# Optimization experiments

Hardware: AMD Instinct MI355X
Metric: run time of the kernel (lower is better)

Reference implementation:

```python
import jax, jax.numpy as jnp
import numpy as np

STATE_DIM = 512
HIDDEN = 256
ACTION = 8
BATCH = 32768
LN_EPS = 1e-5


def setup_inputs() -> dict:
    key = jax.random.key(0)
    ks = jax.random.split(key, 24)
    s = 0.02
    inp = {
        'initial_state': jax.random.normal(ks[0], (BATCH, STATE_DIM), jnp.float32),
        'final_state': jax.random.normal(ks[1], (BATCH, STATE_DIM), jnp.float32),
        'horizon': 10,
        # fc: Linear(1024->256), LayerNorm(256), ReLU, Linear(256->256), ReLU
        'W1': jax.random.normal(ks[2], (HIDDEN, 2 * STATE_DIM), jnp.float32) * s,
        'b1': jnp.zeros((HIDDEN,), jnp.float32),
        'ln_g': jnp.ones((HIDDEN,), jnp.float32),
        'ln_b': jnp.zeros((HIDDEN,), jnp.float32),
        'W2': jax.random.normal(ks[3], (HIDDEN, HIDDEN), jnp.float32) * s,
        'b2': jnp.zeros((HIDDEN,), jnp.float32),
        # GRU layer 0 (input=ACTION) and layer 1 (input=HIDDEN)
        'Wih0': jax.random.normal(ks[4], (3 * HIDDEN, ACTION), jnp.float32) * s,
        'Whh0': jax.random.normal(ks[5], (3 * HIDDEN, HIDDEN), jnp.float32) * s,
        'bih0': jnp.zeros((3 * HIDDEN,), jnp.float32),
        'bhh0': jnp.zeros((3 * HIDDEN,), jnp.float32),
        'Wih1': jax.random.normal(ks[6], (3 * HIDDEN, HIDDEN), jnp.float32) * s,
        'Whh1': jax.random.normal(ks[7], (3 * HIDDEN, HIDDEN), jnp.float32) * s,
        'bih1': jnp.zeros((3 * HIDDEN,), jnp.float32),
        'bhh1': jnp.zeros((3 * HIDDEN,), jnp.float32),
        # fc_action: 256 -> 8
        'Wa': jax.random.normal(ks[8], (ACTION, HIDDEN), jnp.float32) * s,
        'ba': jnp.zeros((ACTION,), jnp.float32),
        # fc_init_hidden: 256 -> 512
        'Winit': jax.random.normal(ks[9], (2 * HIDDEN, HIDDEN), jnp.float32) * s,
        'binit': jnp.zeros((2 * HIDDEN,), jnp.float32),
    }
    return inp


def _gru_cell(x, h, Wih, Whh, bih, bhh):
    # torch.nn.GRU cell: gates ordered [r, z, n]
    gi = x @ Wih.T + bih              # [B, 3H]
    gh = h @ Whh.T + bhh              # [B, 3H]
    i_r, i_z, i_n = jnp.split(gi, 3, axis=-1)
    h_r, h_z, h_n = jnp.split(gh, 3, axis=-1)
    r = jax.nn.sigmoid(i_r + h_r)
    z = jax.nn.sigmoid(i_z + h_z)
    n = jnp.tanh(i_n + r * h_n)
    return (1.0 - z) * n + z * h


def reference(initial_state, final_state, horizon, W1, b1, ln_g, ln_b, W2, b2,
              Wih0, Whh0, bih0, bhh0, Wih1, Whh1, bih1, bhh1, Wa, ba, Winit, binit):
    B = initial_state.shape[0]
    combined = jnp.concatenate([initial_state, final_state], axis=-1)  # [B, 2*state]
    h = combined @ W1.T + b1
    mu = jnp.mean(h, axis=-1, keepdims=True)
    var = jnp.var(h, axis=-1, keepdims=True)
    h = (h - mu) * jax.lax.rsqrt(var + LN_EPS) * ln_g + ln_b
    h = jax.nn.relu(h)
    h = jax.nn.relu(h @ W2.T + b2)    # [B, H]

    # Replicates torch .view(2, B, H) on a [B, 2H] tensor (row-major reshape)
    hidden = jnp.reshape(h @ Winit.T + binit, (2, B, HIDDEN))
    h0, h1 = hidden[0], hidden[1]
    a0 = jnp.zeros((B, ACTION), initial_state.dtype)

    def step(carry, _):
        h0, h1, a = carry
        h0n = _gru_cell(a, h0, Wih0, Whh0, bih0, bhh0)
        h1n = _gru_cell(h0n, h1, Wih1, Whh1, bih1, bhh1)
        logits = h1n @ Wa.T + ba       # [B, A]
        a_next = jax.nn.softmax(logits, axis=-1)
        return (h0n, h1n, a_next), logits

    _, logits_seq = jax.lax.scan(step, (h0, h1, a0), None, length=horizon)
    return jnp.transpose(logits_seq, (1, 0, 2))  # [B, horizon, A]
```

## Files before the change

### kernel.cpp

```cpp
#include <hip/hip_runtime.h>


#define HS 264
#define HR 256

typedef __attribute__((ext_vector_type(8))) short short8;
typedef __attribute__((ext_vector_type(4))) float fvec4;

__device__ __forceinline__ float bf2f(unsigned short u) {
    union { unsigned int u; float f; } x; x.u = ((unsigned int)u) << 16; return x.f;
}
__device__ __forceinline__ unsigned short f2bf(float f) {
    union { float f; unsigned int u; } x; x.f = f;
    unsigned int r = x.u + 0x7fffu + ((x.u >> 16) & 1u);
    return (unsigned short)(r >> 16);
}
__device__ __forceinline__ float sigm(float x)   { return __builtin_amdgcn_rcpf(1.f + __expf(-x)); }
__device__ __forceinline__ float tanh_f(float x) { return 2.f * __builtin_amdgcn_rcpf(1.f + __expf(-2.f * x)) - 1.f; }

__device__ __forceinline__ short8 ld8(const unsigned short* p) {
    return *reinterpret_cast<const short8*>(p);
}
__device__ __forceinline__ fvec4 mfma16(short8 a, short8 b, fvec4 c) {
    return __builtin_amdgcn_mfma_f32_16x16x32_bf16(a, b, c, 0, 0, 0);
}
__device__ __forceinline__ fvec4 splat4(float v) {
    fvec4 r = {v, v, v, v}; return r;
}
__device__ __forceinline__ int swz(int row, int k) {
    return row * HR + (k ^ ((row & 7) << 3));
}

__device__ __forceinline__ int packoff(int e, int K) {
    const int n = e / K, k = e % K;
    return (((n >> 4) * (K >> 5) + (k >> 5)) << 9)
         + (((((k >> 3) & 3) << 4) | (n & 15)) << 3) + (k & 7);
}

__global__ __launch_bounds__(256) void k_prep(
    const float* __restrict__ W1, const float* __restrict__ W2,
    const float* __restrict__ Winit, const float* __restrict__ Wih0,
    const float* __restrict__ Whh0, const float* __restrict__ Wih1,
    const float* __restrict__ Whh1, const float* __restrict__ Wa,
    unsigned short* __restrict__ wb)
{
    int i = blockIdx.x * 256 + threadIdx.x;
    if (i >= 1056768) return;
    float v; int dst;
    if (i < 262144) {
        v = W1[i];                dst = packoff(i, 1024);
    } else if (i < 327680) {
        int e = i - 262144;  v = W2[e];    dst = 262144 + packoff(e, 256);
    } else if (i < 458752) {
        int e = i - 327680;  v = Winit[e]; dst = 327680 + packoff(e, 256);
    } else if (i < 464896) {
        v = Wih0[i - 458752];     dst = i;
    } else if (i < 661504) {
        int e = i - 464896;  v = Whh0[e];  dst = 464896 + packoff(e, 256);
    } else if (i < 858112) {
        int e = i - 661504;  v = Wih1[e];  dst = 661504 + packoff(e, 256);
    } else if (i < 1054720) {
        int e = i - 858112;  v = Whh1[e];  dst = 858112 + packoff(e, 256);
    } else {
        v = Wa[i - 1054720];      dst = i;
    }
    wb[dst] = f2bf(v);
}

__global__ __launch_bounds__(512, 2) void k_encode(
    const float* __restrict__ ini, const float* __restrict__ fin,
    const unsigned short* __restrict__ W1b, const float* __restrict__ b1,
    const float* __restrict__ lng, const float* __restrict__ lnb,
    const unsigned short* __restrict__ W2b, const float* __restrict__ b2,
    const unsigned short* __restrict__ Winitb, const float* __restrict__ binit,
    unsigned short* __restrict__ h0g, unsigned short* __restrict__ h1g)
{
    __shared__ unsigned short hb[64 * HS];
    __shared__ unsigned short at[2][64 * 40];
    __shared__ float ps[64][8][2];
    __shared__ float st[64][2];
    const int tid = threadIdx.x, lane = tid & 63, w = tid >> 6;
    const int l15 = lane & 15, q = lane >> 4;
    const int rows0 = blockIdx.x * 64;
    const int c0 = w * 32;
    const fvec4 fz = {0.f, 0.f, 0.f, 0.f};

    const int srow = tid >> 3, sseg = (tid & 7) * 4;

    fvec4 acc[4][2];
#pragma unroll
    for (int rt = 0; rt < 4; ++rt) { acc[rt][0] = fz; acc[rt][1] = fz; }
    {
        const float* src0 = ini + (rows0 + srow) * 512 + sseg;
        fvec4 v = *reinterpret_cast<const fvec4*>(src0);
        union { unsigned short s[4]; unsigned long long u; } p;
        p.s[0] = f2bf(v[0]); p.s[1] = f2bf(v[1]); p.s[2] = f2bf(v[2]); p.s[3] = f2bf(v[3]);
        *reinterpret_cast<unsigned long long*>(&at[0][srow * 40 + sseg]) = p.u;
    }
    __syncthreads();
#pragma unroll 1
    for (int kc = 0; kc < 32; ++kc) {
        const int buf = kc & 1;
        if (kc < 31) {
            const int k0 = (kc + 1) * 32 + sseg;
            const float* src = (k0 < 512) ? (ini + (rows0 + srow) * 512 + k0)
                                          : (fin + (rows0 + srow) * 512 + (k0 - 512));
            fvec4 v = *reinterpret_cast<const fvec4*>(src);
            union { unsigned short s[4]; unsigned long long u; } p;
            p.s[0] = f2bf(v[0]); p.s[1] = f2bf(v[1]); p.s[2] = f2bf(v[2]); p.s[3] = f2bf(v[3]);
            *reinterpret_cast<unsigned long long*>(&at[buf ^ 1][srow * 40 + sseg]) = p.u;
        }
        short8 b8a = ld8(W1b + (((w * 2 + 0) * 32 + kc) * 64 + lane) * 8);
        short8 b8b = ld8(W1b + (((w * 2 + 1) * 32 + kc) * 64 + lane) * 8);
        short8 a8[4];
#pragma unroll
        for (int rt = 0; rt < 4; ++rt)
            a8[rt] = ld8(&at[buf][(rt * 16 + l15) * 40 + q * 8]);
#pragma unroll
        for (int rt = 0; rt < 4; ++rt) {
            acc[rt][0] = mfma16(a8[rt], b8a, acc[rt][0]);
            acc[rt][1] = mfma16(a8[rt], b8b, acc[rt][1]);
        }
        __syncthreads();
    }
    float bv[2] = { b1[c0 + l15], b1[c0 + 16 + l15] };
#pragma unroll
    for (int rt = 0; rt < 4; ++rt)
#pragma unroll
        for (int r = 0; r < 4; ++r) {
            float s = 0.f, s2 = 0.f;
#pragma unroll
            for (int ct = 0; ct < 2; ++ct) {
                float v = acc[rt][ct][r] + bv[ct];
                acc[rt][ct][r] = v;
                s += v; s2 += v * v;
            }
#pragma unroll
            for (int off = 1; off < 16; off <<= 1) {
                s  += __shfl_xor(s,  off, 64);
                s2 += __shfl_xor(s2, off, 64);
            }
            if (l15 == 0) {
                int row = rt * 16 + q * 4 + r;
                ps[row][w][0] = s; ps[row][w][1] = s2;
            }
        }
    __syncthreads();
    if (tid < 64) {
        float s = 0.f, s2 = 0.f;
#pragma unroll
        for (int j = 0; j < 8; ++j) { s += ps[tid][j][0]; s2 += ps[tid][j][1]; }
        float mu = s * (1.f / 256.f);
        float var = s2 * (1.f / 256.f) - mu * mu;
        st[tid][0] = mu; st[tid][1] = rsqrtf(var + 1e-5f);
    }
    __syncthreads();
    {
        float gv[2]  = { lng[c0 + l15], lng[c0 + 16 + l15] };
        float bbv[2] = { lnb[c0 + l15], lnb[c0 + 16 + l15] };
#pragma unroll
        for (int rt = 0; rt < 4; ++rt)
#pragma unroll
            for (int ct = 0; ct < 2; ++ct)
#pragma unroll
                for (int r = 0; r < 4; ++r) {
                    int row = rt * 16 + q * 4 + r;
                    float v = (acc[rt][ct][r] - st[row][0]) * st[row][1] * gv[ct] + bbv[ct];
                    v = fmaxf(v, 0.f);
                    hb[row * HS + c0 + ct * 16 + l15] = f2bf(v);
                }
    }
    __syncthreads();
    fvec4 acc2[4][2];
#pragma unroll
    for (int rt = 0; rt < 4; ++rt) { acc2[rt][0] = fz; acc2[rt][1] = fz; }
#pragma unroll 2
    for (int kc = 0; kc < 8; ++kc) {
        const int k0 = kc * 32 + q * 8;
        short8 a8[4];
#pragma unroll
        for (int rt = 0; rt < 4; ++rt) a8[rt] = ld8(hb + (rt * 16 + l15) * HS + k0);
#pragma unroll
        for (int ct = 0; ct < 2; ++ct) {
            short8 b8 = ld8(W2b + (((w * 2 + ct) * 8 + kc) * 64 + lane) * 8);
#pragma unroll
            for (int rt = 0; rt < 4; ++rt) acc2[rt][ct] = mfma16(a8[rt], b8, acc2[rt][ct]);
        }
    }
    {
        float b2v[2] = { b2[c0 + l15], b2[c0 + 16 + l15] };
        unsigned short stg[4][2][4];
#pragma unroll
        for (int rt = 0; rt < 4; ++rt)
#pragma unroll
            for (int ct = 0; ct < 2; ++ct)
#pragma unroll
                for (int r = 0; r < 4; ++r)
                    stg[rt][ct][r] = f2bf(fmaxf(acc2[rt][ct][r] + b2v[ct], 0.f));
        __syncthreads();
#pragma unroll
        for (int rt = 0; rt < 4; ++rt)
#pragma unroll
            for (int ct = 0; ct < 2; ++ct)
#pragma unroll
                for (int r = 0; r < 4; ++r)
                    hb[(rt * 16 + q * 4 + r) * HS + c0 + ct * 16 + l15] = stg[rt][ct][r];
    }
    __syncthreads();
    fvec4 a3[4][4];
#pragma unroll
    for (int rt = 0; rt < 4; ++rt)
#pragma unroll
        for (int ct = 0; ct < 4; ++ct) a3[rt][ct] = fz;
#pragma unroll 1
    for (int kc = 0; kc < 8; ++kc) {
        const int k0 = kc * 32 + q * 8;
        short8 a8[4];
#pragma unroll
        for (int rt = 0; rt < 4; ++rt) a8[rt] = ld8(hb + (rt * 16 + l15) * HS + k0);
#pragma unroll
        for (int ct = 0; ct < 4; ++ct) {
            short8 b8 = ld8(Winitb + (((w * 4 + ct) * 8 + kc) * 64 + lane) * 8);
#pragma unroll
            for (int rt = 0; rt < 4; ++rt) a3[rt][ct] = mfma16(a8[rt], b8, a3[rt][ct]);
        }
    }
    const int c0i = w * 64;
#pragma unroll
    for (int ct = 0; ct < 4; ++ct) {
        const int j = c0i + ct * 16 + l15;
        const float bz = binit[j];
        const int half = j >> 8, cc = j & 255;
#pragma unroll
        for (int rt = 0; rt < 4; ++rt)
#pragma unroll
            for (int r = 0; r < 4; ++r) {
                const int i = rows0 + rt * 16 + q * 4 + r;
                const unsigned short v = f2bf(a3[rt][ct][r] + bz);
                if (i < 16384) h0g[(2 * i + half) * 256 + cc] = v;
                else           h1g[(2 * (i - 16384) + half) * 256 + cc] = v;
            }
    }
}

__global__ __launch_bounds__(512, 2) void k_roll(
    const unsigned short* __restrict__ h0g, const unsigned short* __restrict__ h1g,
    const unsigned short* __restrict__ Wih0b, const unsigned short* __restrict__ Whh0b,
    const unsigned short* __restrict__ Wih1b, const unsigned short* __restrict__ Whh1b,
    const unsigned short* __restrict__ Wab,
    const float* __restrict__ bih0, const float* __restrict__ bhh0,
    const float* __restrict__ bih1, const float* __restrict__ bhh1,
    const float* __restrict__ ba, float* __restrict__ out)
{
    __shared__ unsigned short h0sb[2][64 * HR];
    __shared__ unsigned short h1sb[2][64 * HR];
    __shared__ unsigned short avs[64 * 8];
    __shared__ float ldsb[2048];
    const int tid = threadIdx.x, lane = tid & 63, w = tid >> 6;
    const int l15 = lane & 15, q = lane >> 4;
    const int rows0 = blockIdx.x * 64;
    const int cb = w * 32;
    const fvec4 fz = {0.f, 0.f, 0.f, 0.f};
    const short8 z8 = {0,0,0,0,0,0,0,0};

    for (int it = tid; it < 64 * 32; it += 512) {
        const int row = it >> 5, g = (it & 31) * 8;
        const int d = swz(row, g);
        *reinterpret_cast<short8*>(&h0sb[0][d]) = ld8(h0g + (rows0 + row) * 256 + g);
        *reinterpret_cast<short8*>(&h1sb[0][d]) = ld8(h1g + (rows0 + row) * 256 + g);
    }
    if (tid < 256) {
        const int j = tid;
        ldsb[j]       = bih0[j] + bhh0[j];
        ldsb[256 + j] = bih0[256 + j] + bhh0[256 + j];
        ldsb[512 + j] = bih0[512 + j];
        ldsb[768 + j] = bhh0[512 + j];
    } else {
        const int j = tid - 256;
        ldsb[1024 + j] = bih1[j] + bhh1[j];
        ldsb[1280 + j] = bih1[256 + j] + bhh1[256 + j];
        ldsb[1536 + j] = bih1[512 + j];
        ldsb[1792 + j] = bhh1[512 + j];
    }
    const float bav = ba[l15 & 7];
    __syncthreads();

    for (int t = 0; t < 10; ++t) {
        const int cur = t & 1, nxt = cur ^ 1;
        const unsigned short* h0c = h0sb[cur];
        unsigned short*       h0n = h0sb[nxt];
        const unsigned short* h1c = h1sb[cur];
        unsigned short*       h1n = h1sb[nxt];
#pragma unroll 1
        for (int p = 0; p < 2; ++p) {
            const int c = cb + p * 16 + l15;
            fvec4 aR[4], aZ[4], aNi[4], aNh[4];
            {
                const float vr = ldsb[c],       vz = ldsb[256 + c];
                const float vi = ldsb[512 + c], vh = ldsb[768 + c];
#pragma unroll
                for (int rt = 0; rt < 4; ++rt) {
                    aR[rt]  = splat4(vr);
                    aZ[rt]  = splat4(vz);
                    aNi[rt] = splat4(vi);
                    aNh[rt] = splat4(vh);
                }
            }
            if (t > 0) {
                const unsigned short* wp = Wih0b + c * 8;
                const short8 wr = ld8(wp);
                const short8 wz = ld8(wp + 2048);
                const short8 wn = ld8(wp + 4096);
#pragma unroll
                for (int rt = 0; rt < 4; ++rt) {
                    short8 v = ld8(avs + (rt * 16 + l15) * 8);
                    const short8 av = (q == 0) ? v : z8;
                    aR[rt]  = mfma16(av, wr, aR[rt]);
                    aZ[rt]  = mfma16(av, wz, aZ[rt]);
                    aNi[rt] = mfma16(av, wn, aNi[rt]);
                }
            }
#pragma unroll 4
            for (int kc = 0; kc < 8; ++kc) {
                const int k0 = kc * 32 + q * 8;
                const unsigned short* wp =
                    Whh0b + ((((w * 2 + p) * 8 + kc) * 64 + lane) * 8);
                const short8 wr = ld8(wp);
                const short8 wz = ld8(wp + 65536);
                const short8 wn = ld8(wp + 131072);
#pragma unroll
                for (int rt = 0; rt < 4; ++rt) {
                    const short8 ah = ld8(h0c + swz(rt * 16 + l15, k0));
                    aR[rt]  = mfma16(ah, wr, aR[rt]);
                    aZ[rt]  = mfma16(ah, wz, aZ[rt]);
                    aNh[rt] = mfma16(ah, wn, aNh[rt]);
                }
            }
#pragma unroll
            for (int rt = 0; rt < 4; ++rt)
#pragma unroll
                for (int r = 0; r < 4; ++r) {
                    const int row = rt * 16 + q * 4 + r;
                    const float hold = bf2f(h0c[swz(row, c)]);
                    const float rr = sigm(aR[rt][r]);
                    const float zz = sigm(aZ[rt][r]);
                    const float nn = tanh_f(aNi[rt][r] + rr * aNh[rt][r]);
                    h0n[swz(row, c)] = f2bf((1.f - zz) * nn + zz * hold);
                }
        }
        __syncthreads();
#pragma unroll 1
        for (int p = 0; p < 2; ++p) {
            const int c = cb + p * 16 + l15;
            fvec4 aR[4], aZ[4], aNi[4], aNh[4];
            {
                const float vr = ldsb[1024 + c], vz = ldsb[1280 + c];
                const float vi = ldsb[1536 + c], vh = ldsb[1792 + c];
#pragma unroll
                for (int rt = 0; rt < 4; ++rt) {
                    aR[rt]  = splat4(vr);
                    aZ[rt]  = splat4(vz);
                    aNi[rt] = splat4(vi);
                    aNh[rt] = splat4(vh);
                }
            }
#pragma unroll 4
            for (int kc = 0; kc < 8; ++kc) {
                const int k0 = kc * 32 + q * 8;
                const unsigned short* wi =
                    Wih1b + ((((w * 2 + p) * 8 + kc) * 64 + lane) * 8);
                const short8 wir = ld8(wi);
                const short8 wiz = ld8(wi + 65536);
                const short8 win = ld8(wi + 131072);
#pragma unroll
                for (int rt = 0; rt < 4; ++rt) {
                    const short8 ai = ld8(h0n + swz(rt * 16 + l15, k0));
                    aR[rt]  = mfma16(ai, wir, aR[rt]);
                    aZ[rt]  = mfma16(ai, wiz, aZ[rt]);
                    aNi[rt] = mfma16(ai, win, aNi[rt]);
                }
            }
#pragma unroll 4
            for (int kc = 0; kc < 8; ++kc) {
                const int k0 = kc * 32 + q * 8;
                const unsigned short* wh =
                    Whh1b + ((((w * 2 + p) * 8 + kc) * 64 + lane) * 8);
                const short8 whr = ld8(wh);
                const short8 whz = ld8(wh + 65536);
                const short8 whn = ld8(wh + 131072);
#pragma unroll
                for (int rt = 0; rt < 4; ++rt) {
                    const short8 ah = ld8(h1c + swz(rt * 16 + l15, k0));
                    aR[rt]  = mfma16(ah, whr, aR[rt]);
                    aZ[rt]  = mfma16(ah, whz, aZ[rt]);
                    aNh[rt] = mfma16(ah, whn, aNh[rt]);
                }
            }
#pragma unroll
            for (int rt = 0; rt < 4; ++rt)
#pragma unroll
                for (int r = 0; r < 4; ++r) {
                    const int row = rt * 16 + q * 4 + r;
                    const float hold = bf2f(h1c[swz(row, c)]);
                    const float rr = sigm(aR[rt][r]);
                    const float zz = sigm(aZ[rt][r]);
                    const float nn = tanh_f(aNi[rt][r] + rr * aNh[rt][r]);
                    h1n[swz(row, c)] = f2bf((1.f - zz) * nn + zz * hold);
                }
        }
        __syncthreads();
        if (w < 4) {
            fvec4 f = fz;
#pragma unroll 1
            for (int kc = 0; kc < 8; ++kc) {
                const int k0 = kc * 32 + q * 8;
                short8 a8 = ld8(h1n + swz(w * 16 + l15, k0));
                short8 b8 = ld8(Wab + (l15 & 7) * 256 + k0);
                f = mfma16(a8, b8, f);
            }
#pragma unroll
            for (int r = 0; r < 4; ++r) {
                float s = f[r] + bav;
                float m = s;
                m = fmaxf(m, __shfl_xor(m, 1, 64));
                m = fmaxf(m, __shfl_xor(m, 2, 64));
                m = fmaxf(m, __shfl_xor(m, 4, 64));
                float e = __expf(s - m);
                float se = e;
                se += __shfl_xor(se, 1, 64);
                se += __shfl_xor(se, 2, 64);
                se += __shfl_xor(se, 4, 64);
                if (l15 < 8) {
                    const int lrow = w * 16 + q * 4 + r;
                    out[(rows0 + lrow) * 80 + t * 8 + l15] = s;
                    avs[lrow * 8 + l15] = f2bf(e * __builtin_amdgcn_rcpf(se));
                }
            }
        }
        __syncthreads();
    }
}

extern "C" void kernel_launch(void* const* d_in, const int* in_sizes, int n_in,
                              void* d_out, int out_size, void* d_ws, size_t ws_size,
                              hipStream_t stream)
{
    const float* ini   = (const float*)d_in[0];
    const float* fin   = (const float*)d_in[1];
    const float* W1    = (const float*)d_in[3];
    const float* b1    = (const float*)d_in[4];
    const float* lng   = (const float*)d_in[5];
    const float* lnb   = (const float*)d_in[6];
    const float* W2    = (const float*)d_in[7];
    const float* b2    = (const float*)d_in[8];
    const float* Wih0  = (const float*)d_in[9];
    const float* Whh0  = (const float*)d_in[10];
    const float* bih0  = (const float*)d_in[11];
    const float* bhh0  = (const float*)d_in[12];
    const float* Wih1  = (const float*)d_in[13];
    const float* Whh1  = (const float*)d_in[14];
    const float* bih1  = (const float*)d_in[15];
    const float* bhh1  = (const float*)d_in[16];
    const float* Wa    = (const float*)d_in[17];
    const float* ba    = (const float*)d_in[18];
    const float* Winit = (const float*)d_in[19];
    const float* binit = (const float*)d_in[20];
    float* out = (float*)d_out;

    char* ws = (char*)d_ws;
    unsigned short* wb     = (unsigned short*)ws;
    unsigned short* W1b    = wb;
    unsigned short* W2b    = wb + 262144;
    unsigned short* Winitb = wb + 327680;
    unsigned short* Wih0b  = wb + 458752;
    unsigned short* Whh0b  = wb + 464896;
    unsigned short* Wih1b  = wb + 661504;
    unsigned short* Whh1b  = wb + 858112;
    unsigned short* Wab    = wb + 1054720;
    unsigned short* h0g = (unsigned short*)(ws + 2113536);
    unsigned short* h1g = (unsigned short*)(ws + 18890752);

    k_prep<<<dim3(4128), dim3(256), 0, stream>>>(W1, W2, Winit, Wih0, Whh0, Wih1, Whh1, Wa, wb);
    k_encode<<<dim3(512), dim3(512), 0, stream>>>(ini, fin, W1b, b1, lng, lnb, W2b, b2,
                                                  Winitb, binit, h0g, h1g);
    k_roll<<<dim3(512), dim3(512), 0, stream>>>(h0g, h1g, Wih0b, Whh0b, Wih1b, Whh1b, Wab,
                                                bih0, bhh0, bih1, bhh1, ba, out);
}
```

Before: 724.1 us.

## Double k_roll waves to 16 per block and use padded LDS rows

The GRU rollout kernel now runs 1024 threads per block, so each wave owns one 16-column slice instead of looping over two. This raises waves per CU for latency hiding and shortens each wave's serial work between barriers. The XOR-swizzled hidden-state LDS layout is replaced by rows padded to 264 elements, which removes the swizzle index arithmetic but may change the bank-conflict pattern. The tighter launch bounds cap registers per thread, which risks spills given the 16 MFMA accumulators each wave holds.

```diff
diff --git a/kernel.cpp b/kernel.cpp
--- a/kernel.cpp
+++ b/kernel.cpp
@@ -2,7 +2,6 @@
 
 
 #define HS 264
-#define HR 256
 
 typedef __attribute__((ext_vector_type(8))) short short8;
 typedef __attribute__((ext_vector_type(4))) float fvec4;
@@ -26,9 +25,6 @@
 }
 __device__ __forceinline__ fvec4 splat4(float v) {
     fvec4 r = {v, v, v, v}; return r;
-}
-__device__ __forceinline__ int swz(int row, int k) {
-    return row * HR + (k ^ ((row & 7) << 3));
 }
 
 __device__ __forceinline__ int packoff(int e, int K) {
@@ -243,7 +239,7 @@
     }
 }
 
-__global__ __launch_bounds__(512, 2) void k_roll(
+__global__ __launch_bounds__(1024, 4) void k_roll(
     const unsigned short* __restrict__ h0g, const unsigned short* __restrict__ h1g,
     const unsigned short* __restrict__ Wih0b, const unsigned short* __restrict__ Whh0b,
     const unsigned short* __restrict__ Wih1b, const unsigned short* __restrict__ Whh1b,
@@ -252,22 +248,21 @@
     const float* __restrict__ bih1, const float* __restrict__ bhh1,
     const float* __restrict__ ba, float* __restrict__ out)
 {
-    __shared__ unsigned short h0sb[2][64 * HR];
-    __shared__ unsigned short h1sb[2][64 * HR];
+    __shared__ unsigned short h0sb[2][64 * HS];
+    __shared__ unsigned short h1sb[2][64 * HS];
     __shared__ unsigned short avs[64 * 8];
     __shared__ float ldsb[2048];
     const int tid = threadIdx.x, lane = tid & 63, w = tid >> 6;
     const int l15 = lane & 15, q = lane >> 4;
     const int rows0 = blockIdx.x * 64;
-    const int cb = w * 32;
+    const int c = w * 16 + l15;
     const fvec4 fz = {0.f, 0.f, 0.f, 0.f};
     const short8 z8 = {0,0,0,0,0,0,0,0};
 
-    for (int it = tid; it < 64 * 32; it += 512) {
+    for (int it = tid; it < 64 * 32; it += 1024) {
         const int row = it >> 5, g = (it & 31) * 8;
-        const int d = swz(row, g);
-        *reinterpret_cast<short8*>(&h0sb[0][d]) = ld8(h0g + (rows0 + row) * 256 + g);
-        *reinterpret_cast<short8*>(&h1sb[0][d]) = ld8(h1g + (rows0 + row) * 256 + g);
+        *reinterpret_cast<short8*>(&h0sb[0][row * HS + g]) = ld8(h0g + (rows0 + row) * 256 + g);
+        *reinterpret_cast<short8*>(&h1sb[0][row * HS + g]) = ld8(h1g + (rows0 + row) * 256 + g);
     }
     if (tid < 256) {
         const int j = tid;
@@ -275,7 +270,7 @@
         ldsb[256 + j] = bih0[256 + j] + bhh0[256 + j];
         ldsb[512 + j] = bih0[512 + j];
         ldsb[768 + j] = bhh0[512 + j];
-    } else {
+    } else if (tid < 512) {
         const int j = tid - 256;
         ldsb[1024 + j] = bih1[j] + bhh1[j];
         ldsb[1280 + j] = bih1[256 + j] + bhh1[256 + j];
@@ -291,9 +286,7 @@
         unsigned short*       h0n = h0sb[nxt];
         const unsigned short* h1c = h1sb[cur];
         unsigned short*       h1n = h1sb[nxt];
-#pragma unroll 1
-        for (int p = 0; p < 2; ++p) {
-            const int c = cb + p * 16 + l15;
+        {
             fvec4 aR[4], aZ[4], aNi[4], aNh[4];
             {
                 const float vr = ldsb[c],       vz = ldsb[256 + c];
@@ -320,17 +313,17 @@
                     aNi[rt] = mfma16(av, wn, aNi[rt]);
                 }
             }
-#pragma unroll 4
+#pragma unroll 2
             for (int kc = 0; kc < 8; ++kc) {
                 const int k0 = kc * 32 + q * 8;
                 const unsigned short* wp =
-                    Whh0b + ((((w * 2 + p) * 8 + kc) * 64 + lane) * 8);
+                    Whh0b + (((w * 8 + kc) * 64 + lane) * 8);
                 const short8 wr = ld8(wp);
                 const short8 wz = ld8(wp + 65536);
                 const short8 wn = ld8(wp + 131072);
 #pragma unroll
                 for (int rt = 0; rt < 4; ++rt) {
-                    const short8 ah = ld8(h0c + swz(rt * 16 + l15, k0));
+                    const short8 ah = ld8(h0c + (rt * 16 + l15) * HS + k0);
                     aR[rt]  = mfma16(ah, wr, aR[rt]);
                     aZ[rt]  = mfma16(ah, wz, aZ[rt]);
                     aNh[rt] = mfma16(ah, wn, aNh[rt]);
@@ -341,17 +334,15 @@
 #pragma unroll
                 for (int r = 0; r < 4; ++r) {
                     const int row = rt * 16 + q * 4 + r;
-                    const float hold = bf2f(h0c[swz(row, c)]);
+                    const float hold = bf2f(h0c[row * HS + c]);
                     const float rr = sigm(aR[rt][r]);
                     const float zz = sigm(aZ[rt][r]);
                     const float nn = tanh_f(aNi[rt][r] + rr * aNh[rt][r]);
-                    h0n[swz(row, c)] = f2bf((1.f - zz) * nn + zz * hold);
+                    h0n[row * HS + c] = f2bf((1.f - zz) * nn + zz * hold);
                 }
         }
         __syncthreads();
-#pragma unroll 1
-        for (int p = 0; p < 2; ++p) {
-            const int c = cb + p * 16 + l15;
+        {
             fvec4 aR[4], aZ[4], aNi[4], aNh[4];
             {
                 const float vr = ldsb[1024 + c], vz = ldsb[1280 + c];
@@ -364,33 +355,33 @@
                     aNh[rt] = splat4(vh);
                 }
             }
-#pragma unroll 4
+#pragma unroll 2
             for (int kc = 0; kc < 8; ++kc) {
                 const int k0 = kc * 32 + q * 8;
                 const unsigned short* wi =
-                    Wih1b + ((((w * 2 + p) * 8 + kc) * 64 + lane) * 8);
+                    Wih1b + (((w * 8 + kc) * 64 + lane) * 8);
                 const short8 wir = ld8(wi);
                 const short8 wiz = ld8(wi + 65536);
                 const short8 win = ld8(wi + 131072);
 #pragma unroll
                 for (int rt = 0; rt < 4; ++rt) {
-                    const short8 ai = ld8(h0n + swz(rt * 16 + l15, k0));
+                    const short8 ai = ld8(h0n + (rt * 16 + l15) * HS + k0);
                     aR[rt]  = mfma16(ai, wir, aR[rt]);
                     aZ[rt]  = mfma16(ai, wiz, aZ[rt]);
                     aNi[rt] = mfma16(ai, win, aNi[rt]);
                 }
             }
-#pragma unroll 4
+#pragma unroll 2
             for (int kc = 0; kc < 8; ++kc) {
                 const int k0 = kc * 32 + q * 8;
                 const unsigned short* wh =
-                    Whh1b + ((((w * 2 + p) * 8 + kc) * 64 + lane) * 8);
+                    Whh1b + (((w * 8 + kc) * 64 + lane) * 8);
                 const short8 whr = ld8(wh);
                 const short8 whz = ld8(wh + 65536);
                 const short8 whn = ld8(wh + 131072);
 #pragma unroll
                 for (int rt = 0; rt < 4; ++rt) {
-                    const short8 ah = ld8(h1c + swz(rt * 16 + l15, k0));
+                    const short8 ah = ld8(h1c + (rt * 16 + l15) * HS + k0);
                     aR[rt]  = mfma16(ah, whr, aR[rt]);
                     aZ[rt]  = mfma16(ah, whz, aZ[rt]);
                     aNh[rt] = mfma16(ah, whn, aNh[rt]);
@@ -401,11 +392,11 @@
 #pragma unroll
                 for (int r = 0; r < 4; ++r) {
                     const int row = rt * 16 + q * 4 + r;
-                    const float hold = bf2f(h1c[swz(row, c)]);
+                    const float hold = bf2f(h1c[row * HS + c]);
                     const float rr = sigm(aR[rt][r]);
                     const float zz = sigm(aZ[rt][r]);
                     const float nn = tanh_f(aNi[rt][r] + rr * aNh[rt][r]);
-                    h1n[swz(row, c)] = f2bf((1.f - zz) * nn + zz * hold);
+                    h1n[row * HS + c] = f2bf((1.f - zz) * nn + zz * hold);
                 }
         }
         __syncthreads();
@@ -414,7 +405,7 @@
 #pragma unroll 1
             for (int kc = 0; kc < 8; ++kc) {
                 const int k0 = kc * 32 + q * 8;
-                short8 a8 = ld8(h1n + swz(w * 16 + l15, k0));
+                short8 a8 = ld8(h1n + (w * 16 + l15) * HS + k0);
                 short8 b8 = ld8(Wab + (l15 & 7) * 256 + k0);
                 f = mfma16(a8, b8, f);
             }
@@ -483,6 +474,6 @@
     k_prep<<<dim3(4128), dim3(256), 0, stream>>>(W1, W2, Winit, Wih0, Whh0, Wih1, Whh1, Wa, wb);
     k_encode<<<dim3(512), dim3(512), 0, stream>>>(ini, fin, W1b, b1, lng, lnb, W2b, b2,
                                                   Winitb, binit, h0g, h1g);
-    k_roll<<<dim3(512), dim3(512), 0, stream>>>(h0g, h1g, Wih0b, Whh0b, Wih1b, Whh1b, Wab,
-                                                bih0, bhh0, bih1, bhh1, ba, out);
-}
+    k_roll<<<dim3(512), dim3(1024), 0, stream>>>(h0g, h1g, Wih0b, Whh0b, Wih1b, Whh1b, Wab,
+                                                 bih0, bhh0, bih1, bhh1, ba, out);
+}
```

Result: faster. 675.1 us (-6.8%).
